# Optimization experiments

Hardware: AMD Instinct MI355X
Metric: run time of the kernel (lower is better)

## Reference

```python
import jax, jax.numpy as jnp
import numpy as np

B, L, D, H = 2, 4096, 768, 12
HS = D // H  # head_size = 64
SCALE = HS ** -0.5


def setup_inputs() -> dict:
    key = jax.random.key(0)
    k1, k2, k3 = jax.random.split(key, 3)
    x = jax.random.normal(k1, (B, L, D), dtype=jnp.float32)
    # torch nn.Linear weights are [out_features, in_features]; y = x @ W.T
    Wq = jax.random.normal(k2, (D, D), dtype=jnp.float32) * (D ** -0.5)
    Wo = jax.random.normal(k3, (D, D), dtype=jnp.float32) * (D ** -0.5)
    return {"x": x, "Wq": Wq, "Wo": Wo}


def reference(x, Wq, Wo):
    b, l, d = x.shape
    # NOTE: source module uses self.query for Q, K, AND V (bug preserved).
    q = jnp.einsum('bld,ed->ble', x, Wq)              # [B,L,D]
    q = q.reshape(b, l, H, HS).transpose(0, 2, 1, 3)   # [B,H,L,HS]
    k = v = q                                          # K = V = Q (faithful)
    scores = jnp.einsum('bhqd,bhkd->bhqk', q, k) * SCALE  # [B,H,L,L]
    attn = jax.nn.softmax(scores, axis=-1)
    out = jnp.einsum('bhqk,bhkd->bhqd', attn, v)       # [B,H,L,HS]
    out = out.transpose(0, 2, 1, 3).reshape(b, l, d)   # [B,L,D]
    out = jnp.einsum('bld,ed->ble', out, Wo)           # output projection
    return out
```

## Files before the change

kernel.cpp:

```cpp
#include <hip/hip_runtime.h>
#include <hip/hip_bf16.h>

#define LQ 4096
#define DQ 768
#define NH 12
#define NB 2

typedef __attribute__((ext_vector_type(8))) short short8;
typedef __attribute__((ext_vector_type(2))) unsigned uint2v;
typedef __attribute__((ext_vector_type(4))) float f32x4;

__device__ __forceinline__ short f2bf(float f) {
    union { float f; unsigned u; } v; v.f = f;
    unsigned r = v.u + 0x7FFFu + ((v.u >> 16) & 1u);
    return (short)(r >> 16);
}

__device__ __forceinline__ unsigned pk2(float a, float b) {
    float2 t; t.x = a; t.y = b;
    __hip_bfloat162 h = __float22bfloat162_rn(t);
    unsigned u; __builtin_memcpy(&u, &h, 4);
    return u;
}

__device__ __forceinline__ f32x4 mfma16(short8 a, short8 b, f32x4 c) {
    return __builtin_amdgcn_mfma_f32_16x16x32_bf16(a, b, c, 0, 0, 0);
}

#define SQRT_C 0.424660891f

__global__ __launch_bounds__(256) void cvtw(const float* __restrict__ a,
                                            short* __restrict__ o) {
    int i = blockIdx.x * 256 + threadIdx.x;
    float4 v = ((const float4*)a)[i];
    *(uint2v*)&o[i * 4] = (uint2v){pk2(v.x, v.y), pk2(v.z, v.w)};
}


template <int MODE>
__global__ __launch_bounds__(256, 3) void gemm_nt(const short* __restrict__ A,
                                                  const short* __restrict__ Wb,
                                                  void* __restrict__ Cp,
                                                  short* __restrict__ Vf) {
    __shared__ short As[128 * 72];
    __shared__ short Bs[64 * 72];
    const int t = threadIdx.x;
    const int lane = t & 63, w = t >> 6;
    const int lr = lane & 15, qd = lane >> 4;
    const int wm = (w & 1) * 64, wn = (w >> 1) * 32;
    const int lin = blockIdx.x;
    const int xcd = lin & 7, jj = lin >> 3;
    const int nt = jj % 12, mt = (jj / 12) * 8 + xcd;
    const int m0 = mt * 128, n0 = nt * 64;

    f32x4 acc[4][2];
#pragma unroll
    for (int i = 0; i < 4; ++i)
#pragma unroll
        for (int j = 0; j < 2; ++j) acc[i][j] = (f32x4){0.f, 0.f, 0.f, 0.f};

#pragma unroll
    for (int u = 0; u < 4; ++u) {
        int c = t + 256 * u, row = c >> 3, col = (c & 7) << 3;
        *(short8*)&As[row * 72 + col] = *(const short8*)&A[(size_t)(m0 + row) * DQ + col];
    }
#pragma unroll
    for (int u = 0; u < 2; ++u) {
        int c = t + 256 * u, row = c >> 3, col = (c & 7) << 3;
        *(short8*)&Bs[row * 72 + col] = *(const short8*)&Wb[(size_t)(n0 + row) * DQ + col];
    }
    __syncthreads();

    for (int kt = 0; kt < 12; ++kt) {
        short8 ra[4], rb[2];
        if (kt < 11) {
            const int k0 = (kt + 1) * 64;
#pragma unroll
            for (int u = 0; u < 4; ++u) {
                int c = t + 256 * u, row = c >> 3, col = (c & 7) << 3;
                ra[u] = *(const short8*)&A[(size_t)(m0 + row) * DQ + k0 + col];
            }
#pragma unroll
            for (int u = 0; u < 2; ++u) {
                int c = t + 256 * u, row = c >> 3, col = (c & 7) << 3;
                rb[u] = *(const short8*)&Wb[(size_t)(n0 + row) * DQ + k0 + col];
            }
        }
#pragma unroll
        for (int s = 0; s < 2; ++s) {
            short8 af[4], bf[2];
#pragma unroll
            for (int i = 0; i < 4; ++i)
                af[i] = *(short8*)&As[(wm + 16 * i + lr) * 72 + 32 * s + qd * 8];
#pragma unroll
            for (int j = 0; j < 2; ++j)
                bf[j] = *(short8*)&Bs[(wn + 16 * j + lr) * 72 + 32 * s + qd * 8];
#pragma unroll
            for (int i = 0; i < 4; ++i)
#pragma unroll
                for (int j = 0; j < 2; ++j)
                    acc[i][j] = mfma16(af[i], bf[j], acc[i][j]);
        }
        if (kt < 11) {
            __syncthreads();
#pragma unroll
            for (int u = 0; u < 4; ++u) {
                int c = t + 256 * u, row = c >> 3, col = (c & 7) << 3;
                *(short8*)&As[row * 72 + col] = ra[u];
            }
#pragma unroll
            for (int u = 0; u < 2; ++u) {
                int c = t + 256 * u, row = c >> 3, col = (c & 7) << 3;
                *(short8*)&Bs[row * 72 + col] = rb[u];
            }
            __syncthreads();
        }
    }

    if (MODE == 0) {
#pragma unroll
        for (int i = 0; i < 4; ++i)
#pragma unroll
            for (int j = 0; j < 2; ++j) {
                const int row0 = m0 + wm + 16 * i + qd * 4;
                const int col = n0 + wn + 16 * j + lr;
#pragma unroll
                for (int r = 0; r < 4; ++r)
                    ((float*)Cp)[(size_t)(row0 + r) * DQ + col] = acc[i][j][r];
            }
    } else {
        short* Qf = (short*)Cp;
        short* F = As;
        const int bh = (m0 >> 12) * NH + nt;
        const size_t gbase = (size_t)bh * (LQ * 64) + (size_t)(((m0 & 4095) >> 6) << 12);
        __syncthreads();
#pragma unroll
        for (int i = 0; i < 4; ++i)
#pragma unroll
            for (int j = 0; j < 2; ++j) {
                const int kl = wm + 16 * i + qd * 4;
                const int hs = wn + 16 * j + lr;
                const int fi = ((kl >> 6) << 12) + ((((hs >> 4) << 1) + ((kl >> 5) & 1)) << 9)
                             + (((hs & 15) + (((kl >> 3) & 3) << 4)) << 3) + (kl & 7);
                *(uint2v*)&F[fi] = (uint2v){pk2(acc[i][j][0], acc[i][j][1]),
                                            pk2(acc[i][j][2], acc[i][j][3])};
            }
        __syncthreads();
#pragma unroll
        for (int p = 0; p < 4; ++p) {
            int u = t + 256 * p;
            *(short8*)&Vf[gbase + (size_t)u * 8] = *(short8*)&F[u * 8];
        }
        __syncthreads();
#pragma unroll
        for (int i = 0; i < 4; ++i)
#pragma unroll
            for (int j = 0; j < 2; ++j) {
                const int hs = wn + 16 * j + lr;
#pragma unroll
                for (int r = 0; r < 4; ++r) {
                    const int key = wm + 16 * i + qd * 4 + r;
                    const int fi = ((key >> 6) << 12) + (((((key >> 4) & 3) << 1) + (hs >> 5)) << 9)
                                 + (((qd * 4 + r) + (((hs >> 3) & 3) << 4)) << 3) + (hs & 7);
                    F[fi] = f2bf(acc[i][j][r] * SQRT_C);
                }
            }
        __syncthreads();
#pragma unroll
        for (int p = 0; p < 4; ++p) {
            int u = t + 256 * p;
            *(short8*)&Qf[gbase + (size_t)u * 8] = *(short8*)&F[u * 8];
        }
    }
}

__global__ __launch_bounds__(256, 3) void attn(const short* __restrict__ Qf,
                                               const short* __restrict__ Vf,
                                               short* __restrict__ O) {
    const int linear = blockIdx.x;
    const int xcd = linear & 7, slot = linear >> 3;
    const int bh = 3 * xcd + (slot >> 5);
    const int qtile = slot & 31;
    const int t = threadIdx.x;
    const int lane = t & 63, w = t >> 6;
    const int qw = w & 1, half = w >> 1;
    const int lr = lane & 15, qd = lane >> 4;

    __shared__ alignas(16) char smem[43008];
    short* aqs = (short*)smem;
    short* Ps = (short*)(smem + 16384) + w * 2560;

    const short* Qbh = Qf + (size_t)bh * (LQ * 64);
    const short* Vbh = Vf + (size_t)bh * (LQ * 64);
    const int q0 = qtile * 128 + qw * 64;
    const int kb0 = half * 64;

    const short one_bf = (short)0x3F80;
    short8 ones;
#pragma unroll
    for (int j = 0; j < 8; ++j) ones[j] = one_bf;

#pragma unroll
    for (int p = 0; p < 4; ++p) {
        int off = (t + 256 * p) * 8;
        *(short8*)&aqs[off] = *(const short8*)&Qbh[(size_t)qtile * 8192 + off];
    }
    __syncthreads();

    f32x4 oacc[4][4], lacc[4];
#pragma unroll
    for (int i = 0; i < 4; ++i) {
        lacc[i] = (f32x4){0.f, 0.f, 0.f, 0.f};
#pragma unroll
        for (int t2 = 0; t2 < 4; ++t2) oacc[i][t2] = (f32x4){0.f, 0.f, 0.f, 0.f};
    }

    const int aqbase = qw * 4096 + lane * 8;

    short8 kf[2][2];
#pragma unroll
    for (int t4 = 0; t4 < 2; ++t4)
#pragma unroll
        for (int s = 0; s < 2; ++s)
            kf[t4][s] = *(const short8*)&Qbh[kb0 * 2048 + (t4 * 2 + s) * 512 + lane * 8];

    for (int kb = kb0; kb < kb0 + 64; ++kb) {
        short8 vb[4];
#pragma unroll
        for (int t2 = 0; t2 < 4; ++t2)
            vb[t2] = *(const short8*)&Vbh[(kb >> 1) * 4096 + (kb & 1) * 512 + t2 * 1024 + lane * 8];

#pragma unroll
        for (int i = 0; i < 4; ++i) {
            short8 aq0 = *(const short8*)&aqs[aqbase + i * 1024];
            short8 aq1 = *(const short8*)&aqs[aqbase + i * 1024 + 512];
            f32x4 s0 = (f32x4){0.f, 0.f, 0.f, 0.f};
            f32x4 s1 = (f32x4){0.f, 0.f, 0.f, 0.f};
            s0 = mfma16(kf[0][0], aq0, s0);
            s0 = mfma16(kf[0][1], aq1, s0);
            s1 = mfma16(kf[1][0], aq0, s1);
            s1 = mfma16(kf[1][1], aq1, s1);
            *(uint2v*)&Ps[i * 640 + lr * 40 + 4 * qd] =
                (uint2v){pk2(__builtin_amdgcn_exp2f(s0[0]), __builtin_amdgcn_exp2f(s0[1])),
                         pk2(__builtin_amdgcn_exp2f(s0[2]), __builtin_amdgcn_exp2f(s0[3]))};
            *(uint2v*)&Ps[i * 640 + lr * 40 + 16 + 4 * qd] =
                (uint2v){pk2(__builtin_amdgcn_exp2f(s1[0]), __builtin_amdgcn_exp2f(s1[1])),
                         pk2(__builtin_amdgcn_exp2f(s1[2]), __builtin_amdgcn_exp2f(s1[3]))};
        }

        short8 kfn[2][2];
#pragma unroll
        for (int t4 = 0; t4 < 2; ++t4)
#pragma unroll
            for (int s = 0; s < 2; ++s)
                kfn[t4][s] = *(const short8*)&Qbh[(kb + 1) * 2048 + (t4 * 2 + s) * 512 + lane * 8];

#pragma unroll
        for (int i = 0; i < 4; ++i) {
            short8 pa = *(short8*)&Ps[i * 640 + lr * 40 + qd * 8];
#pragma unroll
            for (int t2 = 0; t2 < 4; ++t2)
                oacc[i][t2] = mfma16(pa, vb[t2], oacc[i][t2]);
            lacc[i] = mfma16(pa, ones, lacc[i]);
        }

#pragma unroll
        for (int t4 = 0; t4 < 2; ++t4)
#pragma unroll
            for (int s = 0; s < 2; ++s) kf[t4][s] = kfn[t4][s];
    }

    __syncthreads();
    f32x4* ex = (f32x4*)smem + (qw * 64 + lane) * 21;
    if (half) {
#pragma unroll
        for (int i = 0; i < 4; ++i) {
#pragma unroll
            for (int t2 = 0; t2 < 4; ++t2) ex[i * 4 + t2] = oacc[i][t2];
            ex[16 + i] = lacc[i];
        }
    }
    __syncthreads();
    if (half) return;

#pragma unroll
    for (int i = 0; i < 4; ++i) {
#pragma unroll
        for (int t2 = 0; t2 < 4; ++t2) oacc[i][t2] += ex[i * 4 + t2];
        lacc[i] += ex[16 + i];
    }

    const int b = bh / NH, h = bh % NH;
#pragma unroll
    for (int i = 0; i < 4; ++i) {
        float inv[4];
#pragma unroll
        for (int r = 0; r < 4; ++r) inv[r] = 1.0f / lacc[i][r];
#pragma unroll
        for (int t2 = 0; t2 < 4; ++t2)
#pragma unroll
            for (int r = 0; r < 4; ++r) {
                int lq = q0 + 16 * i + qd * 4 + r;
                int e = h * 64 + 16 * t2 + lr;
                O[((size_t)(b * LQ + lq)) * DQ + e] = f2bf(oacc[i][t2][r] * inv[r]);
            }
    }
}

extern "C" void kernel_launch(void* const* d_in, const int* in_sizes, int n_in,
                              void* d_out, int out_size, void* d_ws, size_t ws_size,
                              hipStream_t stream) {
    (void)in_sizes; (void)n_in; (void)out_size; (void)ws_size;
    const float* x  = (const float*)d_in[0];
    const float* Wq = (const float*)d_in[1];
    const float* Wo = (const float*)d_in[2];
    float* out = (float*)d_out;

    const size_t NQ = (size_t)NB * NH * LQ * 64;
    const size_t NW = (size_t)DQ * DQ;
    short* Qf  = (short*)d_ws;
    short* Vfb = Qf + NQ;
    short* Ows = Vfb + NQ;
    short* Wqb = Ows + (size_t)NB * LQ * DQ;
    short* Wob = Wqb + NW;

    cvtw<<<(NB * LQ * DQ) / 1024, 256, 0, stream>>>(x, Ows);
    cvtw<<<NW / 1024, 256, 0, stream>>>(Wq, Wqb);
    cvtw<<<NW / 1024, 256, 0, stream>>>(Wo, Wob);
    gemm_nt<1><<<768, 256, 0, stream>>>(Ows, Wqb, Qf, Vfb);
    attn<<<768, 256, 0, stream>>>(Qf, Vfb, Ows);
    gemm_nt<0><<<768, 256, 0, stream>>>(Ows, Wob, out, nullptr);
}
```

Before: 241.1 us.

## Use direct global-to-LDS loads with double buffering and XOR swizzle in GEMM

```diff
diff --git a/kernel.cpp b/kernel.cpp
--- a/kernel.cpp
+++ b/kernel.cpp
@@ -27,6 +27,12 @@
     return __builtin_amdgcn_mfma_f32_16x16x32_bf16(a, b, c, 0, 0, 0);
 }
 
+__device__ __forceinline__ void gld16(const short* g, short* l) {
+    __builtin_amdgcn_global_load_lds(
+        (const __attribute__((address_space(1))) unsigned int*)(g),
+        (__attribute__((address_space(3))) unsigned int*)(l), 16, 0, 0);
+}
+
 #define SQRT_C 0.424660891f
 
 __global__ __launch_bounds__(256) void cvtw(const float* __restrict__ a,
@@ -42,8 +48,8 @@
                                                   const short* __restrict__ Wb,
                                                   void* __restrict__ Cp,
                                                   short* __restrict__ Vf) {
-    __shared__ short As[128 * 72];
-    __shared__ short Bs[64 * 72];
+    __shared__ __attribute__((aligned(16))) short As[2][128 * 64];
+    __shared__ __attribute__((aligned(16))) short Bs[2][64 * 64];
     const int t = threadIdx.x;
     const int lane = t & 63, w = t >> 6;
     const int lr = lane & 15, qd = lane >> 4;
@@ -53,6 +59,20 @@
     const int nt = jj % 12, mt = (jj / 12) * 8 + xcd;
     const int m0 = mt * 128, n0 = nt * 64;
 
+    int aoffs[4], boffs[2];
+#pragma unroll
+    for (int u = 0; u < 4; ++u) {
+        int c = (u * 4 + w) * 64 + lane;
+        int row = c >> 3, k = (c & 7) ^ (row & 7);
+        aoffs[u] = (m0 + row) * DQ + k * 8;
+    }
+#pragma unroll
+    for (int u = 0; u < 2; ++u) {
+        int c = (u * 4 + w) * 64 + lane;
+        int row = c >> 3, k = (c & 7) ^ (row & 7);
+        boffs[u] = (n0 + row) * DQ + k * 8;
+    }
+
     f32x4 acc[4][2];
 #pragma unroll
     for (int i = 0; i < 4; ++i)
@@ -60,61 +80,38 @@
         for (int j = 0; j < 2; ++j) acc[i][j] = (f32x4){0.f, 0.f, 0.f, 0.f};
 
 #pragma unroll
-    for (int u = 0; u < 4; ++u) {
-        int c = t + 256 * u, row = c >> 3, col = (c & 7) << 3;
-        *(short8*)&As[row * 72 + col] = *(const short8*)&A[(size_t)(m0 + row) * DQ + col];
-    }
-#pragma unroll
-    for (int u = 0; u < 2; ++u) {
-        int c = t + 256 * u, row = c >> 3, col = (c & 7) << 3;
-        *(short8*)&Bs[row * 72 + col] = *(const short8*)&Wb[(size_t)(n0 + row) * DQ + col];
-    }
+    for (int u = 0; u < 4; ++u) gld16(&A[aoffs[u]], &As[0][(u * 4 + w) * 512]);
+#pragma unroll
+    for (int u = 0; u < 2; ++u) gld16(&Wb[boffs[u]], &Bs[0][(u * 4 + w) * 512]);
     __syncthreads();
 
+    int cur = 0;
     for (int kt = 0; kt < 12; ++kt) {
-        short8 ra[4], rb[2];
         if (kt < 11) {
             const int k0 = (kt + 1) * 64;
 #pragma unroll
-            for (int u = 0; u < 4; ++u) {
-                int c = t + 256 * u, row = c >> 3, col = (c & 7) << 3;
-                ra[u] = *(const short8*)&A[(size_t)(m0 + row) * DQ + k0 + col];
-            }
-#pragma unroll
-            for (int u = 0; u < 2; ++u) {
-                int c = t + 256 * u, row = c >> 3, col = (c & 7) << 3;
-                rb[u] = *(const short8*)&Wb[(size_t)(n0 + row) * DQ + k0 + col];
-            }
+            for (int u = 0; u < 4; ++u) gld16(&A[aoffs[u] + k0], &As[cur ^ 1][(u * 4 + w) * 512]);
+#pragma unroll
+            for (int u = 0; u < 2; ++u) gld16(&Wb[boffs[u] + k0], &Bs[cur ^ 1][(u * 4 + w) * 512]);
         }
 #pragma unroll
         for (int s = 0; s < 2; ++s) {
+            const int cq = ((4 * s + qd) ^ (lr & 7)) * 8;
             short8 af[4], bf[2];
 #pragma unroll
             for (int i = 0; i < 4; ++i)
-                af[i] = *(short8*)&As[(wm + 16 * i + lr) * 72 + 32 * s + qd * 8];
+                af[i] = *(short8*)&As[cur][(wm + 16 * i + lr) * 64 + cq];
 #pragma unroll
             for (int j = 0; j < 2; ++j)
-                bf[j] = *(short8*)&Bs[(wn + 16 * j + lr) * 72 + 32 * s + qd * 8];
+                bf[j] = *(short8*)&Bs[cur][(wn + 16 * j + lr) * 64 + cq];
 #pragma unroll
             for (int i = 0; i < 4; ++i)
 #pragma unroll
                 for (int j = 0; j < 2; ++j)
                     acc[i][j] = mfma16(af[i], bf[j], acc[i][j]);
         }
-        if (kt < 11) {
-            __syncthreads();
-#pragma unroll
-            for (int u = 0; u < 4; ++u) {
-                int c = t + 256 * u, row = c >> 3, col = (c & 7) << 3;
-                *(short8*)&As[row * 72 + col] = ra[u];
-            }
-#pragma unroll
-            for (int u = 0; u < 2; ++u) {
-                int c = t + 256 * u, row = c >> 3, col = (c & 7) << 3;
-                *(short8*)&Bs[row * 72 + col] = rb[u];
-            }
-            __syncthreads();
-        }
+        __syncthreads();
+        cur ^= 1;
     }
 
     if (MODE == 0) {
@@ -130,10 +127,9 @@
             }
     } else {
         short* Qf = (short*)Cp;
-        short* F = As;
+        short* F = (short*)As;
         const int bh = (m0 >> 12) * NH + nt;
         const size_t gbase = (size_t)bh * (LQ * 64) + (size_t)(((m0 & 4095) >> 6) << 12);
-        __syncthreads();
 #pragma unroll
         for (int i = 0; i < 4; ++i)
 #pragma unroll
@@ -217,18 +213,13 @@
 
     const int aqbase = qw * 4096 + lane * 8;
 
-    short8 kf[2][2];
-#pragma unroll
-    for (int t4 = 0; t4 < 2; ++t4)
-#pragma unroll
-        for (int s = 0; s < 2; ++s)
-            kf[t4][s] = *(const short8*)&Qbh[kb0 * 2048 + (t4 * 2 + s) * 512 + lane * 8];
-
     for (int kb = kb0; kb < kb0 + 64; ++kb) {
-        short8 vb[4];
-#pragma unroll
-        for (int t2 = 0; t2 < 4; ++t2)
-            vb[t2] = *(const short8*)&Vbh[(kb >> 1) * 4096 + (kb & 1) * 512 + t2 * 1024 + lane * 8];
+        short8 kf[2][2];
+#pragma unroll
+        for (int t4 = 0; t4 < 2; ++t4)
+#pragma unroll
+            for (int s = 0; s < 2; ++s)
+                kf[t4][s] = *(const short8*)&Qbh[kb * 2048 + (t4 * 2 + s) * 512 + lane * 8];
 
 #pragma unroll
         for (int i = 0; i < 4; ++i) {
@@ -248,12 +239,10 @@
                          pk2(__builtin_amdgcn_exp2f(s1[2]), __builtin_amdgcn_exp2f(s1[3]))};
         }
 
-        short8 kfn[2][2];
-#pragma unroll
-        for (int t4 = 0; t4 < 2; ++t4)
-#pragma unroll
-            for (int s = 0; s < 2; ++s)
-                kfn[t4][s] = *(const short8*)&Qbh[(kb + 1) * 2048 + (t4 * 2 + s) * 512 + lane * 8];
+        short8 vb[4];
+#pragma unroll
+        for (int t2 = 0; t2 < 4; ++t2)
+            vb[t2] = *(const short8*)&Vbh[(kb >> 1) * 4096 + (kb & 1) * 512 + t2 * 1024 + lane * 8];
 
 #pragma unroll
         for (int i = 0; i < 4; ++i) {
@@ -263,11 +252,6 @@
                 oacc[i][t2] = mfma16(pa, vb[t2], oacc[i][t2]);
             lacc[i] = mfma16(pa, ones, lacc[i]);
         }
-
-#pragma unroll
-        for (int t4 = 0; t4 < 2; ++t4)
-#pragma unroll
-            for (int s = 0; s < 2; ++s) kf[t4][s] = kfn[t4][s];
     }
 
     __syncthreads();
```

After: 233.4 us. 3.2% less time.
